# Performance work log

Hardware: AMD Instinct MI355X
Metric: run time of the kernel (lower is better)

Reference implementation:

```python
import jax, jax.numpy as jnp
import numpy as np
from jax import lax

B, H, W = 64, 64, 64
N_CHANNELS = 16
N_FILTERS = 128
N_DENSE = 256
T_STEPS = 60  # update_time() with Tmin=60, Tmax=61


def setup_inputs() -> dict:
    key = jax.random.key(0)
    ks = jax.random.split(key, 7)
    s_conv = 1.0 / np.sqrt(3 * 3 * N_CHANNELS)
    s_d1 = 1.0 / np.sqrt(N_FILTERS)
    s_d2 = 1.0 / np.sqrt(N_DENSE)
    return {
        "input": jax.random.uniform(ks[0], (B, H, W), dtype=jnp.float32),
        # conv kernel in HWIO layout for lax.conv_general_dilated
        "conv_w": jax.random.uniform(ks[1], (3, 3, N_CHANNELS, N_FILTERS), jnp.float32, -s_conv, s_conv),
        "conv_b": jax.random.uniform(ks[2], (N_FILTERS,), jnp.float32, -s_conv, s_conv),
        "w1": jax.random.uniform(ks[3], (N_FILTERS, N_DENSE), jnp.float32, -s_d1, s_d1),
        "b1": jax.random.uniform(ks[4], (N_DENSE,), jnp.float32, -s_d1, s_d1),
        "w2": jax.random.uniform(ks[5], (N_DENSE, N_CHANNELS), jnp.float32, -s_d2, s_d2),
        "b2": jax.random.uniform(ks[6], (N_CHANNELS,), jnp.float32, -s_d2, s_d2),
    }


def reference(input, conv_w, conv_b, w1, b1, w2, b2):
    # grid: (B,H,W,C), channel 0 seeded with the input image
    grid = jnp.zeros((B, H, W, N_CHANNELS), dtype=input.dtype)
    grid = grid.at[..., 0].set(input)
    # zero channel 0 of the delta (channel 0 is frozen)
    ch_mask = (jnp.arange(N_CHANNELS) != 0).astype(input.dtype)  # (C,)

    def step(g, _):
        conv = lax.conv_general_dilated(
            g, conv_w, window_strides=(1, 1), padding="SAME",
            dimension_numbers=("NHWC", "HWIO", "NHWC")) + conv_b
        h = jax.nn.relu(conv)                       # (B,H,W,F)
        d = jax.nn.relu(h @ w1 + b1) @ w2 + b2      # (B,H,W,C)
        alive = (g[..., 0:1] > 0.1).astype(g.dtype)  # (B,H,W,1)
        g = g + d * ch_mask * alive
        return g, None

    grid, _ = lax.scan(step, grid, None, length=T_STEPS)
    return jax.nn.softmax(grid[..., 1:11], axis=-1)  # (B,H,W,10)
```

## Files before the change

kernel.cpp:

```cpp
#include <hip/hip_runtime.h>
#include <math.h>

typedef _Float16 f16;
typedef f16  f16x8 __attribute__((ext_vector_type(8)));
typedef f16  f16x4 __attribute__((ext_vector_type(4)));
typedef float f32x4 __attribute__((ext_vector_type(4)));

#define NB 64
#define NC 16
#define NF 128
#define ND 256
#define NSTEP 60
#define GRID_ELEMS (NB*64*64*NC)
#define NPIX (NB*64*64)

#define KCONV 160
#define HSS   136
#define RPS   18

#define OFF_CW 0
#define OFF_W1 20480
#define OFF_W2 53248

__global__ void init_grid(const float* __restrict__ inp, float* __restrict__ g) {
    int i = blockIdx.x * 256 + threadIdx.x;
    if (i >= GRID_ELEMS) return;
    int c = i & 15;
    g[i] = (c == 0) ? inp[i >> 4] : 0.0f;
}

__global__ void prep_weights(const float* __restrict__ cw, const float* __restrict__ w1,
                             const float* __restrict__ w2, f16* __restrict__ wb) {
    int i = blockIdx.x * 256 + threadIdx.x;
    float v; int off, idx;
    if (i < 20480) {
        int f = i / 160, k = i - f * 160;
        v = (k < 144) ? cw[k * 128 + f] : 0.0f;
        off = OFF_CW; idx = i;
    } else if (i < 20480 + 32768) {
        int r = i - 20480;
        int j = r >> 7, f = r & 127;
        v = w1[f * 256 + j];
        off = OFF_W1; idx = r;
    } else {
        int r = i - 20480 - 32768;
        int c = r >> 8, j = r & 255;
        v = w2[j * 16 + c];
        off = OFF_W2; idx = r;
    }
    wb[off + idx] = (f16)v;
}

__global__ __launch_bounds__(256, 3) void nca_step(
    const float* __restrict__ gin, float* __restrict__ gout,
    const f16* __restrict__ wb,
    const float* __restrict__ cb, const float* __restrict__ b1, const float* __restrict__ b2)
{
    __shared__ f16 smem[21312];
    f16* const hs   = smem;
    f16* const halo = smem + 18432;
    float* const redF = (float*)smem;

    const int t    = threadIdx.x;
    const int w    = t >> 6;
    const int lane = t & 63;
    const int q    = lane >> 4;
    const int l16  = lane & 15;

    const int d  = blockIdx.x;
    const int kk = d >> 3;
    const int b  = ((d & 7) << 3) | (kk >> 5);
    const int tl = kk & 31;
    const int y0 = (tl >> 2) << 3;
    const int x0 = (tl & 3) << 4;

    const float* gb  = gin  + (size_t)b * 64 * 64 * 16;
    float*       gob = gout + (size_t)b * 64 * 64 * 16;

    const int fbase = w << 5;
    f16x8 cA[2][5];
    #pragma unroll
    for (int ft = 0; ft < 2; ++ft)
        #pragma unroll
        for (int kc = 0; kc < 5; ++kc)
            cA[ft][kc] = *(const f16x8*)(wb + OFF_CW +
                (size_t)(fbase + ft * 16 + l16) * KCONV + kc * 32 + q * 8);

    for (int i = t; i < 720; i += 256) {
        int c4 = (i & 3) << 2;
        int xy = i >> 2;
        int xx = xy % 18;
        int yy = xy / 18;
        int gy = y0 + yy - 1, gx = x0 + xx - 1;
        f32x4 v = {0.f, 0.f, 0.f, 0.f};
        if ((unsigned)gy < 64u && (unsigned)gx < 64u)
            v = *(const f32x4*)(gb + (gy * 64 + gx) * 16 + c4);
        f16x4 hv;
        hv.x = (f16)v.x; hv.y = (f16)v.y; hv.z = (f16)v.z; hv.w = (f16)v.w;
        *(f16x4*)(halo + xy * 16 + c4) = hv;
    }
    __syncthreads();

    {
        f32x4 acc[2][8];
        #pragma unroll
        for (int ft = 0; ft < 2; ++ft) {
            f32x4 bias;
            bias.x = cb[fbase + ft * 16 + q * 4 + 0];
            bias.y = cb[fbase + ft * 16 + q * 4 + 1];
            bias.z = cb[fbase + ft * 16 + q * 4 + 2];
            bias.w = cb[fbase + ft * 16 + q * 4 + 3];
            #pragma unroll
            for (int p = 0; p < 8; ++p) acc[ft][p] = bias;
        }

        #pragma unroll
        for (int kc = 0; kc < 5; ++kc) {
            int tap = kc * 2 + (q >> 1);
            if (tap > 8) tap = 8;
            int dy = tap / 3, dx = tap - dy * 3;
            #pragma unroll
            for (int p = 0; p < 8; ++p) {
                int hy = p + dy;
                int hx = l16 + dx;
                f16x8 bf = *(const f16x8*)(halo + (hy * 18 + hx) * 16 + (q & 1) * 8);
                #pragma unroll
                for (int ft = 0; ft < 2; ++ft)
                    acc[ft][p] = __builtin_amdgcn_mfma_f32_16x16x32_f16(cA[ft][kc], bf, acc[ft][p], 0, 0, 0);
            }
        }

        #pragma unroll
        for (int ft = 0; ft < 2; ++ft)
            #pragma unroll
            for (int p = 0; p < 8; ++p) {
                f32x4 a = acc[ft][p];
                f16x4 pk;
                pk.x = (f16)fmaxf(a.x, 0.0f);
                pk.y = (f16)fmaxf(a.y, 0.0f);
                pk.z = (f16)fmaxf(a.z, 0.0f);
                pk.w = (f16)fmaxf(a.w, 0.0f);
                *(f16x4*)(hs + (p * 16 + l16) * HSS + fbase + ft * 16 + q * 4) = pk;
            }
    }
    __syncthreads();

    const int jbase = w << 6;
    f16x8 dA[2][2][4];
    float b1v[2][2][4];
    #pragma unroll
    for (int jp = 0; jp < 2; ++jp)
        #pragma unroll
        for (int jt2 = 0; jt2 < 2; ++jt2) {
            #pragma unroll
            for (int kc = 0; kc < 4; ++kc)
                dA[jp][jt2][kc] = *(const f16x8*)(wb + OFF_W1 +
                    (size_t)(jbase + jp * 32 + jt2 * 16 + l16) * 128 + kc * 32 + q * 8);
            #pragma unroll
            for (int r = 0; r < 4; ++r)
                b1v[jp][jt2][r] = b1[jbase + jp * 32 + jt2 * 16 + q * 4 + r];
        }
    f16x4 w2k[4];
    #pragma unroll
    for (int jt = 0; jt < 4; ++jt)
        w2k[jt] = *(const f16x4*)(wb + OFF_W2 + (size_t)l16 * 256 + jbase + jt * 16 + q * 4);

    f32x4 dacc[8];
    #pragma unroll
    for (int p = 0; p < 8; ++p) { dacc[p].x = 0.f; dacc[p].y = 0.f; dacc[p].z = 0.f; dacc[p].w = 0.f; }

    for (int p = 0; p < 8; ++p) {
        f16x8 hB[4];
        #pragma unroll
        for (int kc = 0; kc < 4; ++kc)
            hB[kc] = *(const f16x8*)(hs + (p * 16 + l16) * HSS + kc * 32 + q * 8);

        #pragma unroll
        for (int jp = 0; jp < 2; ++jp)
            #pragma unroll
            for (int jt2 = 0; jt2 < 2; ++jt2) {
                f32x4 a1;
                a1.x = b1v[jp][jt2][0]; a1.y = b1v[jp][jt2][1];
                a1.z = b1v[jp][jt2][2]; a1.w = b1v[jp][jt2][3];
                #pragma unroll
                for (int kc = 0; kc < 4; ++kc)
                    a1 = __builtin_amdgcn_mfma_f32_16x16x32_f16(dA[jp][jt2][kc], hB[kc], a1, 0, 0, 0);
                f16x4 pk;
                pk.x = (f16)fmaxf(a1.x, 0.0f);
                pk.y = (f16)fmaxf(a1.y, 0.0f);
                pk.z = (f16)fmaxf(a1.z, 0.0f);
                pk.w = (f16)fmaxf(a1.w, 0.0f);
                dacc[p] = __builtin_amdgcn_mfma_f32_16x16x16f16(pk, w2k[jp * 2 + jt2], dacc[p], 0, 0, 0);
            }
    }

    __syncthreads();
    #pragma unroll
    for (int p = 0; p < 8; ++p)
        #pragma unroll
        for (int r = 0; r < 4; ++r) {
            int px = p * 16 + q * 4 + r;
            redF[(w * 128 + px) * RPS + l16] = dacc[p][r];
        }
    __syncthreads();

    {
        const int px  = t >> 1;
        const int ch0 = (t & 1) << 3;
        const int yy = px >> 4, xx = px & 15;
        const size_t pixb = ((size_t)(y0 + yy) * 64 + (x0 + xx)) * 16;
        const float a0 = gb[pixb];
        const bool alive = (a0 > 0.1f);
        #pragma unroll
        for (int h = 0; h < 2; ++h) {
            const int ch = ch0 + h * 4;
            f32x4 v0 = *(const f32x4*)(redF + (0 * 128 + px) * RPS + ch);
            f32x4 v1 = *(const f32x4*)(redF + (1 * 128 + px) * RPS + ch);
            f32x4 v2 = *(const f32x4*)(redF + (2 * 128 + px) * RPS + ch);
            f32x4 v3 = *(const f32x4*)(redF + (3 * 128 + px) * RPS + ch);
            f32x4 sv = v0 + v1 + v2 + v3;
            f32x4 gv = *(const f32x4*)(gb + pixb + ch);
            f32x4 ov;
            #pragma unroll
            for (int i = 0; i < 4; ++i) {
                int c = ch + i;
                float nv = gv[i];
                if (alive && c != 0) nv += sv[i] + b2[c];
                ov[i] = nv;
            }
            *(f32x4*)(gob + pixb + ch) = ov;
        }
    }
}

__global__ void softmax_out(const float* __restrict__ g, float* __restrict__ out) {
    int pix = blockIdx.x * 256 + threadIdx.x;
    if (pix >= NPIX) return;
    const float* gp = g + (size_t)pix * 16;
    float v[10];
    float m = -1e30f;
    #pragma unroll
    for (int i = 0; i < 10; ++i) { v[i] = gp[1 + i]; m = fmaxf(m, v[i]); }
    float s = 0.f;
    #pragma unroll
    for (int i = 0; i < 10; ++i) { v[i] = __expf(v[i] - m); s += v[i]; }
    float inv = 1.0f / s;
    float* op = out + (size_t)pix * 10;
    #pragma unroll
    for (int i = 0; i < 10; ++i) op[i] = v[i] * inv;
}

extern "C" void kernel_launch(void* const* d_in, const int* in_sizes, int n_in,
                              void* d_out, int out_size, void* d_ws, size_t ws_size,
                              hipStream_t stream) {
    const float* inp = (const float*)d_in[0];
    const float* cw  = (const float*)d_in[1];
    const float* cb  = (const float*)d_in[2];
    const float* w1  = (const float*)d_in[3];
    const float* b1  = (const float*)d_in[4];
    const float* w2  = (const float*)d_in[5];
    const float* b2  = (const float*)d_in[6];
    float* out = (float*)d_out;

    float* g0 = (float*)d_ws;
    float* g1 = g0 + GRID_ELEMS;
    f16* wb = (f16*)d_out;

    prep_weights<<<224, 256, 0, stream>>>(cw, w1, w2, wb);
    init_grid<<<(GRID_ELEMS + 255) / 256, 256, 0, stream>>>(inp, g0);

    float* bufs[2] = { g0, g1 };
    for (int s = 0; s < NSTEP; ++s) {
        nca_step<<<2048, 256, 0, stream>>>(bufs[s & 1], bufs[(s + 1) & 1],
                                           wb, cb, b1, b2);
    }
    softmax_out<<<(NPIX + 255) / 256, 256, 0, stream>>>(g0, out);
}
```

Measured before the change: 2.695 ms.

## Split work by pixel rows per wave instead of by filters/dense units

Each wave now owns two pixel rows of the tile and computes all 128 conv filters and all 256 dense units for them, instead of splitting filters and dense units across waves. This removes the cross-wave shared-memory reduction of dense outputs, the extra barriers, and the reduction buffer, and lets the output be written straight from registers. It also raises the occupancy target to 4 blocks per CU. In exchange, every wave now streams the full conv and dense weight sets from global/L2 memory instead of holding a quarter of them in registers, which raises weight load traffic per block.

```diff
diff --git a/kernel.cpp b/kernel.cpp
--- a/kernel.cpp
+++ b/kernel.cpp
@@ -16,7 +16,6 @@
 
 #define KCONV 160
 #define HSS   136
-#define RPS   18
 
 #define OFF_CW 0
 #define OFF_W1 20480
@@ -51,15 +50,14 @@
     wb[off + idx] = (f16)v;
 }
 
-__global__ __launch_bounds__(256, 3) void nca_step(
+__global__ __launch_bounds__(256, 4) void nca_step(
     const float* __restrict__ gin, float* __restrict__ gout,
     const f16* __restrict__ wb,
     const float* __restrict__ cb, const float* __restrict__ b1, const float* __restrict__ b2)
 {
-    __shared__ f16 smem[21312];
+    __shared__ f16 smem[20288];
     f16* const hs   = smem;
-    f16* const halo = smem + 18432;
-    float* const redF = (float*)smem;
+    f16* const halo = smem + 17408;
 
     const int t    = threadIdx.x;
     const int w    = t >> 6;
@@ -76,15 +74,6 @@
 
     const float* gb  = gin  + (size_t)b * 64 * 64 * 16;
     float*       gob = gout + (size_t)b * 64 * 64 * 16;
-
-    const int fbase = w << 5;
-    f16x8 cA[2][5];
-    #pragma unroll
-    for (int ft = 0; ft < 2; ++ft)
-        #pragma unroll
-        for (int kc = 0; kc < 5; ++kc)
-            cA[ft][kc] = *(const f16x8*)(wb + OFF_CW +
-                (size_t)(fbase + ft * 16 + l16) * KCONV + kc * 32 + q * 8);
 
     for (int i = t; i < 720; i += 256) {
         int c4 = (i & 3) << 2;
@@ -101,134 +90,116 @@
     }
     __syncthreads();
 
-    {
-        f32x4 acc[2][8];
-        #pragma unroll
-        for (int ft = 0; ft < 2; ++ft) {
-            f32x4 bias;
-            bias.x = cb[fbase + ft * 16 + q * 4 + 0];
-            bias.y = cb[fbase + ft * 16 + q * 4 + 1];
-            bias.z = cb[fbase + ft * 16 + q * 4 + 2];
-            bias.w = cb[fbase + ft * 16 + q * 4 + 3];
+    const int pr = w << 1;
+
+    f32x4 acc[8][2];
+    #pragma unroll
+    for (int ft = 0; ft < 8; ++ft) {
+        f32x4 bias = *(const f32x4*)(cb + ft * 16 + q * 4);
+        acc[ft][0] = bias;
+        acc[ft][1] = bias;
+    }
+
+    #pragma unroll
+    for (int kc = 0; kc < 5; ++kc) {
+        f16x8 cA[8];
+        #pragma unroll
+        for (int ft = 0; ft < 8; ++ft)
+            cA[ft] = *(const f16x8*)(wb + OFF_CW +
+                (size_t)(ft * 16 + l16) * KCONV + kc * 32 + q * 8);
+        int tap = kc * 2 + (q >> 1);
+        if (tap > 8) tap = 8;
+        int dy = tap / 3, dx = tap - dy * 3;
+        #pragma unroll
+        for (int pp = 0; pp < 2; ++pp) {
+            int hy = pr + pp + dy;
+            int hx = l16 + dx;
+            f16x8 bf = *(const f16x8*)(halo + (hy * 18 + hx) * 16 + (q & 1) * 8);
             #pragma unroll
-            for (int p = 0; p < 8; ++p) acc[ft][p] = bias;
-        }
-
-        #pragma unroll
-        for (int kc = 0; kc < 5; ++kc) {
-            int tap = kc * 2 + (q >> 1);
-            if (tap > 8) tap = 8;
-            int dy = tap / 3, dx = tap - dy * 3;
-            #pragma unroll
-            for (int p = 0; p < 8; ++p) {
-                int hy = p + dy;
-                int hx = l16 + dx;
-                f16x8 bf = *(const f16x8*)(halo + (hy * 18 + hx) * 16 + (q & 1) * 8);
-                #pragma unroll
-                for (int ft = 0; ft < 2; ++ft)
-                    acc[ft][p] = __builtin_amdgcn_mfma_f32_16x16x32_f16(cA[ft][kc], bf, acc[ft][p], 0, 0, 0);
-            }
-        }
-
-        #pragma unroll
-        for (int ft = 0; ft < 2; ++ft)
-            #pragma unroll
-            for (int p = 0; p < 8; ++p) {
-                f32x4 a = acc[ft][p];
-                f16x4 pk;
-                pk.x = (f16)fmaxf(a.x, 0.0f);
-                pk.y = (f16)fmaxf(a.y, 0.0f);
-                pk.z = (f16)fmaxf(a.z, 0.0f);
-                pk.w = (f16)fmaxf(a.w, 0.0f);
-                *(f16x4*)(hs + (p * 16 + l16) * HSS + fbase + ft * 16 + q * 4) = pk;
-            }
-    }
-    __syncthreads();
-
-    const int jbase = w << 6;
-    f16x8 dA[2][2][4];
-    float b1v[2][2][4];
-    #pragma unroll
-    for (int jp = 0; jp < 2; ++jp)
-        #pragma unroll
-        for (int jt2 = 0; jt2 < 2; ++jt2) {
+            for (int ft = 0; ft < 8; ++ft)
+                acc[ft][pp] = __builtin_amdgcn_mfma_f32_16x16x32_f16(cA[ft], bf, acc[ft][pp], 0, 0, 0);
+        }
+    }
+
+    #pragma unroll
+    for (int pp = 0; pp < 2; ++pp)
+        #pragma unroll
+        for (int ft = 0; ft < 8; ++ft) {
+            f32x4 a = acc[ft][pp];
+            f16x4 pk;
+            pk.x = (f16)fmaxf(a.x, 0.0f);
+            pk.y = (f16)fmaxf(a.y, 0.0f);
+            pk.z = (f16)fmaxf(a.z, 0.0f);
+            pk.w = (f16)fmaxf(a.w, 0.0f);
+            *(f16x4*)(hs + ((pr + pp) * 16 + l16) * HSS + ft * 16 + q * 4) = pk;
+        }
+
+    f16x8 hB[2][4];
+    #pragma unroll
+    for (int pp = 0; pp < 2; ++pp)
+        #pragma unroll
+        for (int kc = 0; kc < 4; ++kc)
+            hB[pp][kc] = *(const f16x8*)(hs + ((pr + pp) * 16 + l16) * HSS + kc * 32 + q * 8);
+
+    float gv[2][4], a0v[2][4];
+    #pragma unroll
+    for (int pp = 0; pp < 2; ++pp)
+        #pragma unroll
+        for (int r = 0; r < 4; ++r) {
+            const int y = y0 + pr + pp;
+            const int x = x0 + q * 4 + r;
+            const size_t pixb = ((size_t)y * 64 + x) * 16;
+            a0v[pp][r] = gb[pixb];
+            gv[pp][r]  = gb[pixb + l16];
+        }
+    const float b2v = b2[l16];
+
+    f32x4 daccA[2], daccB[2];
+    #pragma unroll
+    for (int pp = 0; pp < 2; ++pp) {
+        daccA[pp].x = 0.f; daccA[pp].y = 0.f; daccA[pp].z = 0.f; daccA[pp].w = 0.f;
+        daccB[pp].x = 0.f; daccB[pp].y = 0.f; daccB[pp].z = 0.f; daccB[pp].w = 0.f;
+    }
+
+    auto dense_jt = [&](int jt, f32x4* dst) {
+        f32x4 b1v = *(const f32x4*)(b1 + jt * 16 + q * 4);
+        f16x4 w2f = *(const f16x4*)(wb + OFF_W2 + (size_t)l16 * 256 + jt * 16 + q * 4);
+        f16x8 dAk[4];
+        #pragma unroll
+        for (int kc = 0; kc < 4; ++kc)
+            dAk[kc] = *(const f16x8*)(wb + OFF_W1 +
+                (size_t)(jt * 16 + l16) * 128 + kc * 32 + q * 8);
+        #pragma unroll
+        for (int pp = 0; pp < 2; ++pp) {
+            f32x4 a1 = b1v;
             #pragma unroll
             for (int kc = 0; kc < 4; ++kc)
-                dA[jp][jt2][kc] = *(const f16x8*)(wb + OFF_W1 +
-                    (size_t)(jbase + jp * 32 + jt2 * 16 + l16) * 128 + kc * 32 + q * 8);
-            #pragma unroll
-            for (int r = 0; r < 4; ++r)
-                b1v[jp][jt2][r] = b1[jbase + jp * 32 + jt2 * 16 + q * 4 + r];
-        }
-    f16x4 w2k[4];
-    #pragma unroll
-    for (int jt = 0; jt < 4; ++jt)
-        w2k[jt] = *(const f16x4*)(wb + OFF_W2 + (size_t)l16 * 256 + jbase + jt * 16 + q * 4);
-
-    f32x4 dacc[8];
-    #pragma unroll
-    for (int p = 0; p < 8; ++p) { dacc[p].x = 0.f; dacc[p].y = 0.f; dacc[p].z = 0.f; dacc[p].w = 0.f; }
-
-    for (int p = 0; p < 8; ++p) {
-        f16x8 hB[4];
-        #pragma unroll
-        for (int kc = 0; kc < 4; ++kc)
-            hB[kc] = *(const f16x8*)(hs + (p * 16 + l16) * HSS + kc * 32 + q * 8);
-
-        #pragma unroll
-        for (int jp = 0; jp < 2; ++jp)
-            #pragma unroll
-            for (int jt2 = 0; jt2 < 2; ++jt2) {
-                f32x4 a1;
-                a1.x = b1v[jp][jt2][0]; a1.y = b1v[jp][jt2][1];
-                a1.z = b1v[jp][jt2][2]; a1.w = b1v[jp][jt2][3];
-                #pragma unroll
-                for (int kc = 0; kc < 4; ++kc)
-                    a1 = __builtin_amdgcn_mfma_f32_16x16x32_f16(dA[jp][jt2][kc], hB[kc], a1, 0, 0, 0);
-                f16x4 pk;
-                pk.x = (f16)fmaxf(a1.x, 0.0f);
-                pk.y = (f16)fmaxf(a1.y, 0.0f);
-                pk.z = (f16)fmaxf(a1.z, 0.0f);
-                pk.w = (f16)fmaxf(a1.w, 0.0f);
-                dacc[p] = __builtin_amdgcn_mfma_f32_16x16x16f16(pk, w2k[jp * 2 + jt2], dacc[p], 0, 0, 0);
-            }
-    }
-
-    __syncthreads();
-    #pragma unroll
-    for (int p = 0; p < 8; ++p)
+                a1 = __builtin_amdgcn_mfma_f32_16x16x32_f16(dAk[kc], hB[pp][kc], a1, 0, 0, 0);
+            f16x4 pk;
+            pk.x = (f16)fmaxf(a1.x, 0.0f);
+            pk.y = (f16)fmaxf(a1.y, 0.0f);
+            pk.z = (f16)fmaxf(a1.z, 0.0f);
+            pk.w = (f16)fmaxf(a1.w, 0.0f);
+            dst[pp] = __builtin_amdgcn_mfma_f32_16x16x16f16(pk, w2f, dst[pp], 0, 0, 0);
+        }
+    };
+
+    for (int jh = 0; jh < 8; ++jh) {
+        dense_jt(jh * 2,     daccA);
+        dense_jt(jh * 2 + 1, daccB);
+    }
+
+    #pragma unroll
+    for (int pp = 0; pp < 2; ++pp) {
+        const int y = y0 + pr + pp;
         #pragma unroll
         for (int r = 0; r < 4; ++r) {
-            int px = p * 16 + q * 4 + r;
-            redF[(w * 128 + px) * RPS + l16] = dacc[p][r];
-        }
-    __syncthreads();
-
-    {
-        const int px  = t >> 1;
-        const int ch0 = (t & 1) << 3;
-        const int yy = px >> 4, xx = px & 15;
-        const size_t pixb = ((size_t)(y0 + yy) * 64 + (x0 + xx)) * 16;
-        const float a0 = gb[pixb];
-        const bool alive = (a0 > 0.1f);
-        #pragma unroll
-        for (int h = 0; h < 2; ++h) {
-            const int ch = ch0 + h * 4;
-            f32x4 v0 = *(const f32x4*)(redF + (0 * 128 + px) * RPS + ch);
-            f32x4 v1 = *(const f32x4*)(redF + (1 * 128 + px) * RPS + ch);
-            f32x4 v2 = *(const f32x4*)(redF + (2 * 128 + px) * RPS + ch);
-            f32x4 v3 = *(const f32x4*)(redF + (3 * 128 + px) * RPS + ch);
-            f32x4 sv = v0 + v1 + v2 + v3;
-            f32x4 gv = *(const f32x4*)(gb + pixb + ch);
-            f32x4 ov;
-            #pragma unroll
-            for (int i = 0; i < 4; ++i) {
-                int c = ch + i;
-                float nv = gv[i];
-                if (alive && c != 0) nv += sv[i] + b2[c];
-                ov[i] = nv;
-            }
-            *(f32x4*)(gob + pixb + ch) = ov;
+            const int x = x0 + q * 4 + r;
+            const size_t pixb = ((size_t)y * 64 + x) * 16;
+            float sv = daccA[pp][r] + daccB[pp][r];
+            float nv = gv[pp][r];
+            if (a0v[pp][r] > 0.1f && l16 != 0) nv += sv + b2v;
+            gob[pixb + l16] = nv;
         }
     }
 }
```

Measured after the change: 6.712 ms. 149% more time.

## Cut registers and LDS to fit four blocks per CU in NCA step

Applied to the files above, without the earlier changes.

Raises the launch bound from three to four waves-per-SIMD blocks. To fit, conv weights are now streamed one k-chunk at a time with a one-ahead prefetch, the dense loop processes the hidden units in two passes so fewer W1/W2 fragments stay live, and the reduction stride drops from 18 to 17 floats to shrink LDS. The cost is extra global/L2 weight reloads, loops that are no longer unrolled, and scalar instead of vector LDS reads in the reduction.

```diff
diff --git a/kernel.cpp b/kernel.cpp
--- a/kernel.cpp
+++ b/kernel.cpp
@@ -16,7 +16,7 @@
 
 #define KCONV 160
 #define HSS   136
-#define RPS   18
+#define RPS   17
 
 #define OFF_CW 0
 #define OFF_W1 20480
@@ -51,14 +51,14 @@
     wb[off + idx] = (f16)v;
 }
 
-__global__ __launch_bounds__(256, 3) void nca_step(
+__global__ __launch_bounds__(256, 4) void nca_step(
     const float* __restrict__ gin, float* __restrict__ gout,
     const f16* __restrict__ wb,
     const float* __restrict__ cb, const float* __restrict__ b1, const float* __restrict__ b2)
 {
-    __shared__ f16 smem[21312];
+    __shared__ f16 smem[20288];
     f16* const hs   = smem;
-    f16* const halo = smem + 18432;
+    f16* const halo = smem + 17408;
     float* const redF = (float*)smem;
 
     const int t    = threadIdx.x;
@@ -76,15 +76,6 @@
 
     const float* gb  = gin  + (size_t)b * 64 * 64 * 16;
     float*       gob = gout + (size_t)b * 64 * 64 * 16;
-
-    const int fbase = w << 5;
-    f16x8 cA[2][5];
-    #pragma unroll
-    for (int ft = 0; ft < 2; ++ft)
-        #pragma unroll
-        for (int kc = 0; kc < 5; ++kc)
-            cA[ft][kc] = *(const f16x8*)(wb + OFF_CW +
-                (size_t)(fbase + ft * 16 + l16) * KCONV + kc * 32 + q * 8);
 
     for (int i = t; i < 720; i += 256) {
         int c4 = (i & 3) << 2;
@@ -101,6 +92,7 @@
     }
     __syncthreads();
 
+    const int fbase = w << 5;
     {
         f32x4 acc[2][8];
         #pragma unroll
@@ -114,8 +106,19 @@
             for (int p = 0; p < 8; ++p) acc[ft][p] = bias;
         }
 
-        #pragma unroll
+        f16x8 cAc[2], cAn[2];
+        #pragma unroll
+        for (int ft = 0; ft < 2; ++ft)
+            cAc[ft] = *(const f16x8*)(wb + OFF_CW +
+                (size_t)(fbase + ft * 16 + l16) * KCONV + q * 8);
+
+        #pragma unroll 1
         for (int kc = 0; kc < 5; ++kc) {
+            int kcn = (kc < 4) ? kc + 1 : 4;
+            #pragma unroll
+            for (int ft = 0; ft < 2; ++ft)
+                cAn[ft] = *(const f16x8*)(wb + OFF_CW +
+                    (size_t)(fbase + ft * 16 + l16) * KCONV + kcn * 32 + q * 8);
             int tap = kc * 2 + (q >> 1);
             if (tap > 8) tap = 8;
             int dy = tap / 3, dx = tap - dy * 3;
@@ -124,10 +127,11 @@
                 int hy = p + dy;
                 int hx = l16 + dx;
                 f16x8 bf = *(const f16x8*)(halo + (hy * 18 + hx) * 16 + (q & 1) * 8);
-                #pragma unroll
-                for (int ft = 0; ft < 2; ++ft)
-                    acc[ft][p] = __builtin_amdgcn_mfma_f32_16x16x32_f16(cA[ft][kc], bf, acc[ft][p], 0, 0, 0);
-            }
+                acc[0][p] = __builtin_amdgcn_mfma_f32_16x16x32_f16(cAc[0], bf, acc[0][p], 0, 0, 0);
+                acc[1][p] = __builtin_amdgcn_mfma_f32_16x16x32_f16(cAc[1], bf, acc[1][p], 0, 0, 0);
+            }
+            cAc[0] = cAn[0];
+            cAc[1] = cAn[1];
         }
 
         #pragma unroll
@@ -146,52 +150,50 @@
     __syncthreads();
 
     const int jbase = w << 6;
-    f16x8 dA[2][2][4];
-    float b1v[2][2][4];
-    #pragma unroll
-    for (int jp = 0; jp < 2; ++jp)
+    f32x4 dacc[8];
+    #pragma unroll
+    for (int p = 0; p < 8; ++p) { dacc[p].x = 0.f; dacc[p].y = 0.f; dacc[p].z = 0.f; dacc[p].w = 0.f; }
+
+    #pragma unroll 1
+    for (int jp = 0; jp < 2; ++jp) {
+        f16x8 dA[2][4];
+        float b1v[2][4];
+        f16x4 w2f[2];
         #pragma unroll
         for (int jt2 = 0; jt2 < 2; ++jt2) {
             #pragma unroll
             for (int kc = 0; kc < 4; ++kc)
-                dA[jp][jt2][kc] = *(const f16x8*)(wb + OFF_W1 +
+                dA[jt2][kc] = *(const f16x8*)(wb + OFF_W1 +
                     (size_t)(jbase + jp * 32 + jt2 * 16 + l16) * 128 + kc * 32 + q * 8);
             #pragma unroll
             for (int r = 0; r < 4; ++r)
-                b1v[jp][jt2][r] = b1[jbase + jp * 32 + jt2 * 16 + q * 4 + r];
-        }
-    f16x4 w2k[4];
-    #pragma unroll
-    for (int jt = 0; jt < 4; ++jt)
-        w2k[jt] = *(const f16x4*)(wb + OFF_W2 + (size_t)l16 * 256 + jbase + jt * 16 + q * 4);
-
-    f32x4 dacc[8];
-    #pragma unroll
-    for (int p = 0; p < 8; ++p) { dacc[p].x = 0.f; dacc[p].y = 0.f; dacc[p].z = 0.f; dacc[p].w = 0.f; }
-
-    for (int p = 0; p < 8; ++p) {
-        f16x8 hB[4];
-        #pragma unroll
-        for (int kc = 0; kc < 4; ++kc)
-            hB[kc] = *(const f16x8*)(hs + (p * 16 + l16) * HSS + kc * 32 + q * 8);
-
-        #pragma unroll
-        for (int jp = 0; jp < 2; ++jp)
+                b1v[jt2][r] = b1[jbase + jp * 32 + jt2 * 16 + q * 4 + r];
+            w2f[jt2] = *(const f16x4*)(wb + OFF_W2 + (size_t)l16 * 256 + jbase + jp * 32 + jt2 * 16 + q * 4);
+        }
+
+        #pragma unroll
+        for (int p = 0; p < 8; ++p) {
+            f16x8 hB[4];
+            #pragma unroll
+            for (int kc = 0; kc < 4; ++kc)
+                hB[kc] = *(const f16x8*)(hs + (p * 16 + l16) * HSS + kc * 32 + q * 8);
+
             #pragma unroll
             for (int jt2 = 0; jt2 < 2; ++jt2) {
                 f32x4 a1;
-                a1.x = b1v[jp][jt2][0]; a1.y = b1v[jp][jt2][1];
-                a1.z = b1v[jp][jt2][2]; a1.w = b1v[jp][jt2][3];
+                a1.x = b1v[jt2][0]; a1.y = b1v[jt2][1];
+                a1.z = b1v[jt2][2]; a1.w = b1v[jt2][3];
                 #pragma unroll
                 for (int kc = 0; kc < 4; ++kc)
-                    a1 = __builtin_amdgcn_mfma_f32_16x16x32_f16(dA[jp][jt2][kc], hB[kc], a1, 0, 0, 0);
+                    a1 = __builtin_amdgcn_mfma_f32_16x16x32_f16(dA[jt2][kc], hB[kc], a1, 0, 0, 0);
                 f16x4 pk;
                 pk.x = (f16)fmaxf(a1.x, 0.0f);
                 pk.y = (f16)fmaxf(a1.y, 0.0f);
                 pk.z = (f16)fmaxf(a1.z, 0.0f);
                 pk.w = (f16)fmaxf(a1.w, 0.0f);
-                dacc[p] = __builtin_amdgcn_mfma_f32_16x16x16f16(pk, w2k[jp * 2 + jt2], dacc[p], 0, 0, 0);
-            }
+                dacc[p] = __builtin_amdgcn_mfma_f32_16x16x16f16(pk, w2f[jt2], dacc[p], 0, 0, 0);
+            }
+        }
     }
 
     __syncthreads();
@@ -214,18 +216,17 @@
         #pragma unroll
         for (int h = 0; h < 2; ++h) {
             const int ch = ch0 + h * 4;
-            f32x4 v0 = *(const f32x4*)(redF + (0 * 128 + px) * RPS + ch);
-            f32x4 v1 = *(const f32x4*)(redF + (1 * 128 + px) * RPS + ch);
-            f32x4 v2 = *(const f32x4*)(redF + (2 * 128 + px) * RPS + ch);
-            f32x4 v3 = *(const f32x4*)(redF + (3 * 128 + px) * RPS + ch);
-            f32x4 sv = v0 + v1 + v2 + v3;
             f32x4 gv = *(const f32x4*)(gb + pixb + ch);
             f32x4 ov;
             #pragma unroll
             for (int i = 0; i < 4; ++i) {
                 int c = ch + i;
+                float sv = ((redF[(0 * 128 + px) * RPS + c]
+                           + redF[(1 * 128 + px) * RPS + c])
+                           + redF[(2 * 128 + px) * RPS + c])
+                           + redF[(3 * 128 + px) * RPS + c];
                 float nv = gv[i];
-                if (alive && c != 0) nv += sv[i] + b2[c];
+                if (alive && c != 0) nv += sv + b2[c];
                 ov[i] = nv;
             }
             *(f32x4*)(gob + pixb + ch) = ov;
```

Measured after the change: 7.138 ms. +164.8%, slower.
